# Performance work log

Hardware: AMD Instinct MI355X
Metric: run time of the kernel (lower is better)

The kernel has to match this reference:

```python
import jax, jax.numpy as jnp
import numpy as np

C = 256
CQK = C // 8


def setup_inputs() -> dict:
    key = jax.random.key(0)
    ks = jax.random.split(key, 8)
    B, H, W = 4, 64, 64
    inputs = jax.random.normal(ks[0], (B, H, W, C), dtype=jnp.float32)
    s = 1.0 / np.sqrt(C)
    Wq = jax.random.normal(ks[1], (C, CQK), dtype=jnp.float32) * s
    bq = jnp.zeros((CQK,), dtype=jnp.float32)
    Wk = jax.random.normal(ks[2], (C, CQK), dtype=jnp.float32) * s
    bk = jnp.zeros((CQK,), dtype=jnp.float32)
    Wv = jax.random.normal(ks[3], (C, C), dtype=jnp.float32) * s
    bv = jnp.zeros((C,), dtype=jnp.float32)
    gamma = jnp.float32(0.7)  # nonzero so attention branch contributes
    return {"inputs": inputs, "Wq": Wq, "bq": bq, "Wk": Wk, "bk": bk,
            "Wv": Wv, "bv": bv, "gamma": gamma}


def reference(inputs, Wq, bq, Wk, bk, Wv, bv, gamma):
    B, H, W, Cin = inputs.shape
    N = H * W
    x = inputs.reshape(B, N, Cin)
    # 1x1 convs == per-pixel channel matmuls
    q = x @ Wq + bq                      # (B, N, C//8)
    k = x @ Wk + bk                      # (B, N, C//8)
    v = x @ Wv + bv                      # (B, N, C)
    energy = jnp.einsum('bnd,bmd->bnm', q, k)   # (B, N, N), no scale (faithful)
    attn = jax.nn.softmax(energy, axis=-1)
    x_out = jnp.einsum('bnm,bmc->bnc', attn, v)  # (B, N, C)
    out = gamma * x_out.reshape(B, H, W, Cin) + inputs
    return out
```

## Files before the change

kernel.cpp:

```cpp
#include <hip/hip_runtime.h>
#include <hip/hip_bf16.h>

#define B_ 4
#define N_ 4096
#define C_ 256
#define D_ 32
#define LOG2E 1.44269504088896340736f
#define MFMA16 __builtin_amdgcn_mfma_f32_16x16x32_bf16

typedef __attribute__((ext_vector_type(8))) short short8;
typedef __attribute__((ext_vector_type(4))) short short4v;
typedef __attribute__((ext_vector_type(4))) float float4v;

__device__ inline short f2bf_rne(float f) {
  unsigned u = __builtin_bit_cast(unsigned, f);
  u += 0x7FFFu + ((u >> 16) & 1u);
  return (short)(u >> 16);
}
__device__ inline float bf2f(short s) {
  unsigned u = ((unsigned)(unsigned short)s) << 16;
  return __builtin_bit_cast(float, u);
}
__device__ inline float fast_exp2(float x) { return __builtin_amdgcn_exp2f(x); }

__global__ __launch_bounds__(256) void cast_w_kernel(
    const float* __restrict__ Wq, const float* __restrict__ Wk,
    const float* __restrict__ Wv, short* __restrict__ WtF) {
  int i  = blockIdx.x * 256 + threadIdx.x;
  int j  = i & 7;
  int l  = (i >> 3) & 63;
  int ks = (i >> 9) & 7;
  int nb = i >> 12;
  int n  = nb * 16 + (l & 15);
  int k  = ks * 32 + ((l >> 4) << 3) + j;
  float v;
  if (n < 32)      v = Wq[k * 32 + n] * LOG2E;
  else if (n < 64) v = Wk[k * 32 + (n - 32)];
  else             v = Wv[k * 256 + (n - 64)];
  WtF[i] = f2bf_rne(v);
}

__global__ __launch_bounds__(256, 2) void proj_kernel(
    const float* __restrict__ x, const short* __restrict__ WtF,
    const float* __restrict__ bq, const float* __restrict__ bk,
    const float* __restrict__ bv,
    short* __restrict__ qb, short* __restrict__ kF, short* __restrict__ vF) {
  int blk = blockIdx.x;
  int b  = blk >> 7;
  int r0 = (blk & 127) * 32;
  int t  = threadIdx.x;
  int w  = t >> 6;
  int l  = t & 63;
  int lc = l & 15;
  int q4 = l >> 4;

  __shared__ __align__(16) short sA[32][272];
  __shared__ __align__(16) short sV[256][40];
  __shared__ __align__(16) short sK[32][36];

  {
    const float* xb = x + (size_t)(b * N_ + r0) * C_;
#pragma unroll
    for (int ch = 0; ch < 8; ch++) {
      int f   = ch * 256 + t;
      int row = f >> 6;
      int col = (f & 63) * 4;
      float4v v = *(const float4v*)(xb + f * 4);
      short4v s;
      s[0] = f2bf_rne(v[0]); s[1] = f2bf_rne(v[1]);
      s[2] = f2bf_rne(v[2]); s[3] = f2bf_rne(v[3]);
      *(short4v*)(&sA[row][col]) = s;
    }
  }
  __syncthreads();

  float4v acc[10];
#pragma unroll
  for (int i = 0; i < 10; i++) { acc[i][0] = 0.f; acc[i][1] = 0.f; acc[i][2] = 0.f; acc[i][3] = 0.f; }

  const short* wbase = WtF + w * 4096 + l * 8;

#define LOADW(B0, B1, B2, B3, B4, KS)                       \
  B0 = *(const short8*)(wbase + (KS) * 512 + 0 * 16384);    \
  B1 = *(const short8*)(wbase + (KS) * 512 + 1 * 16384);    \
  B2 = *(const short8*)(wbase + (KS) * 512 + 2 * 16384);    \
  B3 = *(const short8*)(wbase + (KS) * 512 + 3 * 16384);    \
  B4 = *(const short8*)(wbase + (KS) * 512 + 4 * 16384);

#define DO_MFMA(A0, A1, B0, B1, B2, B3, B4)                 \
  acc[0] = MFMA16(A0, B0, acc[0], 0, 0, 0);                 \
  acc[1] = MFMA16(A1, B0, acc[1], 0, 0, 0);                 \
  acc[2] = MFMA16(A0, B1, acc[2], 0, 0, 0);                 \
  acc[3] = MFMA16(A1, B1, acc[3], 0, 0, 0);                 \
  acc[4] = MFMA16(A0, B2, acc[4], 0, 0, 0);                 \
  acc[5] = MFMA16(A1, B2, acc[5], 0, 0, 0);                 \
  acc[6] = MFMA16(A0, B3, acc[6], 0, 0, 0);                 \
  acc[7] = MFMA16(A1, B3, acc[7], 0, 0, 0);                 \
  acc[8] = MFMA16(A0, B4, acc[8], 0, 0, 0);                 \
  acc[9] = MFMA16(A1, B4, acc[9], 0, 0, 0);

  short8 wA0, wA1, wA2, wA3, wA4, wB0, wB1, wB2, wB3, wB4;
  LOADW(wA0, wA1, wA2, wA3, wA4, 0)
#pragma unroll
  for (int kk = 0; kk < 8; kk += 2) {
    short8 a00 = *(const short8*)(&sA[lc][kk * 32 + q4 * 8]);
    short8 a01 = *(const short8*)(&sA[16 + lc][kk * 32 + q4 * 8]);
    LOADW(wB0, wB1, wB2, wB3, wB4, kk + 1)
    DO_MFMA(a00, a01, wA0, wA1, wA2, wA3, wA4)
    short8 a10 = *(const short8*)(&sA[lc][(kk + 1) * 32 + q4 * 8]);
    short8 a11 = *(const short8*)(&sA[16 + lc][(kk + 1) * 32 + q4 * 8]);
    LOADW(wA0, wA1, wA2, wA3, wA4, kk + 2)
    DO_MFMA(a10, a11, wB0, wB1, wB2, wB3, wB4)
  }
#undef LOADW
#undef DO_MFMA

  {
    float bias0 = (w < 2) ? bq[w * 16 + lc] * LOG2E : bk[(w - 2) * 16 + lc];
#pragma unroll
    for (int rt = 0; rt < 2; rt++) {
      if (w < 2) {
#pragma unroll
        for (int r = 0; r < 4; r++) {
          int row = rt * 16 + q4 * 4 + r;
          qb[(size_t)(b * N_ + r0 + row) * D_ + w * 16 + lc] =
              f2bf_rne(acc[rt][r] + bias0);
        }
      } else {
#pragma unroll
        for (int r = 0; r < 4; r++) {
          int row = rt * 16 + q4 * 4 + r;
          sK[row][(w - 2) * 16 + lc] = f2bf_rne(acc[rt][r] + bias0);
        }
      }
    }
#pragma unroll
    for (int nbo = 1; nbo < 5; nbo++) {
      float bias = bv[(nbo - 1) * 64 + w * 16 + lc];
#pragma unroll
      for (int rt = 0; rt < 2; rt++) {
        float4v a = acc[nbo * 2 + rt];
        short4v pk;
        pk[0] = f2bf_rne(a[0] + bias); pk[1] = f2bf_rne(a[1] + bias);
        pk[2] = f2bf_rne(a[2] + bias); pk[3] = f2bf_rne(a[3] + bias);
        *(short4v*)(&sV[(nbo - 1) * 64 + w * 16 + lc][rt * 16 + q4 * 4]) = pk;
      }
    }
  }
  __syncthreads();

  int kt  = r0 >> 6;
  int ks0 = (r0 >> 5) & 1;

  {
    size_t tb2 = ((size_t)(b * 64 + kt) * 32 + ks0 * 16) * 512;
    int cb = t >> 4;
#pragma unroll
    for (int k = 0; k < 4; k++) {
      int p = (t & 15) * 4 + k;
      int j = p >> 4, i = p & 15;
      short8 vv = *(const short8*)(&sV[cb * 16 + i][j * 8]);
      *(short8*)(vF + tb2 + (size_t)t * 32 + k * 8) = vv;
    }
  }
  if (t < 128) {
    int fr = t >> 6, ll = t & 63;
    int kv = fr * 16 + (ll & 15), dg = ll >> 4;
    size_t tbk = ((size_t)(b * 64 + kt) * 4 + ks0 * 2) * 512;
    short8 kv8 = *(const short8*)(&sK[kv][dg * 8]);
    *(short8*)(kF + tbk + (size_t)t * 8) = kv8;
  }
}

__global__ __launch_bounds__(512, 4) void flash_partial_kernel(
    const short* __restrict__ qb, const short* __restrict__ kF,
    const short* __restrict__ vF, short* __restrict__ obuf,
    float* __restrict__ lbuf) {
  int blk = blockIdx.x;
  int b  = blk & 3;
  int hb = (blk >> 2) & 1;
  int qt = blk >> 3;
  int r0 = qt * 64;
  int t  = threadIdx.x;
  int w  = t >> 6;
  int l  = t & 63;
  int lc = l & 15;
  int q4 = l >> 4;
  int rq = w & 3;
  bool qkw = (w < 4);

  __shared__ __align__(16) short sP[2][64][72];

  int p = (b * 64 + qt) * 2 + hb;

  short8 qf = *(const short8*)(qb + (size_t)(b * N_ + r0 + rq * 16 + lc) * D_ + q4 * 8);

  const short* kbp = kF + ((size_t)(b * 64 + hb * 32) * 4) * 512 + l * 8;
  const short* vbp = vF + ((size_t)(b * 64 + hb * 32) * 32 + 2 * w) * 512 + l * 8;

  short8 kC0, kC1, kC2, kC3;
  short8 vX00, vX01, vX10, vX11;
  short8 vY00, vY01, vY10, vY11;

  kC0 = *(const short8*)(kbp + 0);
  kC1 = *(const short8*)(kbp + 512);
  kC2 = *(const short8*)(kbp + 1024);
  kC3 = *(const short8*)(kbp + 1536);
  vX00 = *(const short8*)(vbp + 0);
  vX01 = *(const short8*)(vbp + 512);
  vX10 = *(const short8*)(vbp + 8192);
  vX11 = *(const short8*)(vbp + 8704);

  float4v O[8];
#pragma unroll
  for (int i = 0; i < 8; i++) { O[i][0] = 0.f; O[i][1] = 0.f; O[i][2] = 0.f; O[i][3] = 0.f; }
  float l_part = 0.f;

#define K_RELOAD(TI)                                                           \
  { size_t o_ = (size_t)(TI) * 2048;                                           \
    kC0 = *(const short8*)(kbp + o_);                                          \
    kC1 = *(const short8*)(kbp + o_ + 512);                                    \
    kC2 = *(const short8*)(kbp + o_ + 1024);                                   \
    kC3 = *(const short8*)(kbp + o_ + 1536); }

#define QK_STEP(SPB, VALID)                                                    \
  { float4v z; z[0] = 0.f; z[1] = 0.f; z[2] = 0.f; z[3] = 0.f;                 \
    float4v S0 = MFMA16(kC0, qf, z, 0, 0, 0);                                  \
    float4v S1 = MFMA16(kC1, qf, z, 0, 0, 0);                                  \
    float4v S2 = MFMA16(kC2, qf, z, 0, 0, 0);                                  \
    float4v S3 = MFMA16(kC3, qf, z, 0, 0, 0);                                  \
    short* rowp = &sP[SPB][rq * 16 + lc][q4 * 4];                              \
    float ts = 0.f;                                                            \
    { float p0 = fast_exp2(S0[0]), p1 = fast_exp2(S0[1]);                      \
      float p2 = fast_exp2(S0[2]), p3 = fast_exp2(S0[3]);                      \
      ts += (p0 + p1) + (p2 + p3);                                             \
      short4v pk; pk[0] = f2bf_rne(p0); pk[1] = f2bf_rne(p1);                  \
      pk[2] = f2bf_rne(p2); pk[3] = f2bf_rne(p3);                              \
      *(short4v*)(rowp + 0) = pk; }                                            \
    { float p0 = fast_exp2(S1[0]), p1 = fast_exp2(S1[1]);                      \
      float p2 = fast_exp2(S1[2]), p3 = fast_exp2(S1[3]);                      \
      ts += (p0 + p1) + (p2 + p3);                                             \
      short4v pk; pk[0] = f2bf_rne(p0); pk[1] = f2bf_rne(p1);                  \
      pk[2] = f2bf_rne(p2); pk[3] = f2bf_rne(p3);                              \
      *(short4v*)(rowp + 16) = pk; }                                           \
    { float p0 = fast_exp2(S2[0]), p1 = fast_exp2(S2[1]);                      \
      float p2 = fast_exp2(S2[2]), p3 = fast_exp2(S2[3]);                      \
      ts += (p0 + p1) + (p2 + p3);                                             \
      short4v pk; pk[0] = f2bf_rne(p0); pk[1] = f2bf_rne(p1);                  \
      pk[2] = f2bf_rne(p2); pk[3] = f2bf_rne(p3);                              \
      *(short4v*)(rowp + 32) = pk; }                                           \
    { float p0 = fast_exp2(S3[0]), p1 = fast_exp2(S3[1]);                      \
      float p2 = fast_exp2(S3[2]), p3 = fast_exp2(S3[3]);                      \
      ts += (p0 + p1) + (p2 + p3);                                             \
      short4v pk; pk[0] = f2bf_rne(p0); pk[1] = f2bf_rne(p1);                  \
      pk[2] = f2bf_rne(p2); pk[3] = f2bf_rne(p3);                              \
      *(short4v*)(rowp + 48) = pk; }                                           \
    if (VALID) l_part += ts; }

#define PV_STEP(SPB, V00, V01, V10, V11)                                       \
  { _Pragma("unroll")                                                          \
    for (int rt = 0; rt < 4; rt++) {                                           \
      short8 pf0 = *(const short8*)(&sP[SPB][rt * 16 + lc][q4 * 8]);           \
      short8 pf1 = *(const short8*)(&sP[SPB][rt * 16 + lc][32 + q4 * 8]);      \
      O[rt * 2 + 0] = MFMA16(pf0, V00, O[rt * 2 + 0], 0, 0, 0);                \
      O[rt * 2 + 0] = MFMA16(pf1, V10, O[rt * 2 + 0], 0, 0, 0);                \
      O[rt * 2 + 1] = MFMA16(pf0, V01, O[rt * 2 + 1], 0, 0, 0);                \
      O[rt * 2 + 1] = MFMA16(pf1, V11, O[rt * 2 + 1], 0, 0, 0);                \
    } }

  if (qkw) {
    QK_STEP(0, true)
    K_RELOAD(1)
  }
  __syncthreads();

  for (int ti = 0; ti < 32; ti += 2) {
    int n1 = ti + 1;
    int n2 = (ti + 2 < 32) ? ti + 2 : 31;
    bool v2 = (ti + 2 < 32);
    int n3 = (ti + 3 < 32) ? ti + 3 : 31;

    { size_t vo = (size_t)n1 * 16384;
      vY00 = *(const short8*)(vbp + vo);
      vY01 = *(const short8*)(vbp + vo + 512);
      vY10 = *(const short8*)(vbp + vo + 8192);
      vY11 = *(const short8*)(vbp + vo + 8704); }
    if (qkw) {
      QK_STEP(1, true)
      K_RELOAD(n2)
    }
    PV_STEP(0, vX00, vX01, vX10, vX11)
    __syncthreads();

    { size_t vo = (size_t)n2 * 16384;
      vX00 = *(const short8*)(vbp + vo);
      vX01 = *(const short8*)(vbp + vo + 512);
      vX10 = *(const short8*)(vbp + vo + 8192);
      vX11 = *(const short8*)(vbp + vo + 8704); }
    if (qkw) {
      QK_STEP(0, v2)
      K_RELOAD(n3)
    }
    PV_STEP(1, vY00, vY01, vY10, vY11)
    __syncthreads();
  }
#undef K_RELOAD
#undef QK_STEP
#undef PV_STEP

  {
    short* ob = obuf + ((size_t)p * 64 + w * 8) * 256 + l * 4;
#pragma unroll
    for (int a = 0; a < 8; a++) {
      float4v o = O[a];
      short4v pk;
      pk[0] = f2bf_rne(o[0]); pk[1] = f2bf_rne(o[1]);
      pk[2] = f2bf_rne(o[2]); pk[3] = f2bf_rne(o[3]);
      *(short4v*)(ob + a * 256) = pk;
    }
  }
  if (qkw) {
    float l_tot = l_part + __shfl_xor(l_part, 16, 64);
    l_tot += __shfl_xor(l_tot, 32, 64);
    if (q4 == 0) lbuf[(size_t)p * 64 + rq * 16 + lc] = l_tot;
  }
}

__global__ __launch_bounds__(256) void merge_kernel(
    const short* __restrict__ obuf, const float* __restrict__ lbuf,
    const float* __restrict__ xin, const float* __restrict__ gptr,
    float* __restrict__ out) {
  int blk = blockIdx.x;
  int t   = threadIdx.x;
  float g = *gptr;

  __shared__ float sS[32][260];
  __shared__ float sLinv[64];

  const short* o0 = obuf + (size_t)(blk * 2 + 0) * 16384;
  const short* o1 = obuf + (size_t)(blk * 2 + 1) * 16384;
  const float* l0 = lbuf + (size_t)(blk * 2 + 0) * 64;
  const float* l1 = lbuf + (size_t)(blk * 2 + 1) * 64;
  size_t gbase = (size_t)blk * 16384;

  if (t < 64) sLinv[t] = __builtin_amdgcn_rcpf(l0[t] + l1[t]);

#pragma unroll
  for (int h = 0; h < 2; h++) {
#pragma unroll
    for (int j = 0; j < 4; j++) {
      int gdx    = j * 256 + t;
      int chunk  = gdx >> 7;
      int within = gdx & 127;
      int offs   = (chunk * 8 + 4 * h) * 256 + within * 8;
      short8 a8 = *(const short8*)(o0 + offs);
      short8 c8 = *(const short8*)(o1 + offs);
      int s_in  = within >> 5;
      int pos8  = within & 31;
      int rt    = 2 * h + (s_in >> 1);
      int cbo   = s_in & 1;
      int chB   = chunk * 32 + cbo * 16;
#pragma unroll
      for (int e = 0; e < 8; e++) {
        int lane = pos8 * 2 + (e >> 2);
        int r    = e & 3;
        int row  = (rt & 1) * 16 + (lane >> 4) * 4 + r;
        int ch   = chB + (lane & 15);
        sS[row][ch] = bf2f(a8[e]) + bf2f(c8[e]);
      }
    }
    __syncthreads();

#pragma unroll
    for (int j = 0; j < 8; j++) {
      int gdx = j * 1024 + t * 4;
      int row = 32 * h + (gdx >> 8);
      int ch  = gdx & 255;
      float linv = sLinv[row];
      size_t gi = gbase + (size_t)(32 * h) * 256 + gdx;
      float4v xv = *(const float4v*)(xin + gi);
      float4v sv = *(const float4v*)(&sS[row - 32 * h][ch]);
      float4v ov;
#pragma unroll
      for (int e = 0; e < 4; e++) ov[e] = g * (sv[e] * linv) + xv[e];
      *(float4v*)(out + gi) = ov;
    }
    __syncthreads();
  }
}

extern "C" void kernel_launch(void* const* d_in, const int* in_sizes, int n_in,
                              void* d_out, int out_size, void* d_ws, size_t ws_size,
                              hipStream_t stream) {
  const float* x     = (const float*)d_in[0];
  const float* Wq    = (const float*)d_in[1];
  const float* bq    = (const float*)d_in[2];
  const float* Wk    = (const float*)d_in[3];
  const float* bk    = (const float*)d_in[4];
  const float* Wv    = (const float*)d_in[5];
  const float* bv    = (const float*)d_in[6];
  const float* gamma = (const float*)d_in[7];
  float* out = (float*)d_out;

  char* ws = (char*)d_ws;
  short* qb   = (short*)ws;
  short* kF   = (short*)(ws + (1u << 20));
  short* vF   = (short*)(ws + (2u << 20));
  short* WtF  = (short*)(ws + (10u << 20));
  short* obuf = (short*)(ws + (11u << 20));
  float* lbuf = (float*)(ws + (28u << 20));

  hipLaunchKernelGGL(cast_w_kernel,        dim3(320), dim3(256), 0, stream, Wq, Wk, Wv, WtF);
  hipLaunchKernelGGL(proj_kernel,          dim3(512), dim3(256), 0, stream, x, WtF, bq, bk, bv, qb, kF, vF);
  hipLaunchKernelGGL(flash_partial_kernel, dim3(512), dim3(512), 0, stream, qb, kF, vF, obuf, lbuf);
  hipLaunchKernelGGL(merge_kernel,         dim3(256), dim3(256), 0, stream, obuf, lbuf, x, gamma, out);
}
```

Measured before the change: 142.1 us.

## Specialize warps into QK/softmax producers and PV consumers

Splits the 8 waves so waves 0-3 only compute QK scores, exp and the row sums into shared memory, while waves 4-7 only do the PV MFMAs over 64 output channels each (16 accumulators instead of 8). V loads move entirely to the consumer waves and the output layout in obuf changes, so the merge kernel's indexing is updated to match. The aim is to let the softmax/QK work and the PV matmul run concurrently on different waves rather than serialised inside every wave. The cost is doubled accumulator registers in the consumer waves, which can raise register pressure under the 512x4 launch bounds, and a possible load imbalance between the two groups.

```diff
diff --git a/kernel.cpp b/kernel.cpp
--- a/kernel.cpp
+++ b/kernel.cpp
@@ -187,6 +187,7 @@
   int lc = l & 15;
   int q4 = l >> 4;
   int rq = w & 3;
+  int cq = w & 3;
   bool qkw = (w < 4);
 
   __shared__ __align__(16) short sP[2][64][72];
@@ -196,24 +197,27 @@
   short8 qf = *(const short8*)(qb + (size_t)(b * N_ + r0 + rq * 16 + lc) * D_ + q4 * 8);
 
   const short* kbp = kF + ((size_t)(b * 64 + hb * 32) * 4) * 512 + l * 8;
-  const short* vbp = vF + ((size_t)(b * 64 + hb * 32) * 32 + 2 * w) * 512 + l * 8;
+  const short* vbp = vF + ((size_t)(b * 64 + hb * 32) * 32 + cq * 4) * 512 + l * 8;
 
   short8 kC0, kC1, kC2, kC3;
-  short8 vX00, vX01, vX10, vX11;
-  short8 vY00, vY01, vY10, vY11;
-
-  kC0 = *(const short8*)(kbp + 0);
-  kC1 = *(const short8*)(kbp + 512);
-  kC2 = *(const short8*)(kbp + 1024);
-  kC3 = *(const short8*)(kbp + 1536);
-  vX00 = *(const short8*)(vbp + 0);
-  vX01 = *(const short8*)(vbp + 512);
-  vX10 = *(const short8*)(vbp + 8192);
-  vX11 = *(const short8*)(vbp + 8704);
-
-  float4v O[8];
-#pragma unroll
-  for (int i = 0; i < 8; i++) { O[i][0] = 0.f; O[i][1] = 0.f; O[i][2] = 0.f; O[i][3] = 0.f; }
+  short8 vC[8];
+
+  if (qkw) {
+    kC0 = *(const short8*)(kbp + 0);
+    kC1 = *(const short8*)(kbp + 512);
+    kC2 = *(const short8*)(kbp + 1024);
+    kC3 = *(const short8*)(kbp + 1536);
+  } else {
+#pragma unroll
+    for (int ks = 0; ks < 2; ks++)
+#pragma unroll
+      for (int cb = 0; cb < 4; cb++)
+        vC[ks * 4 + cb] = *(const short8*)(vbp + ks * 8192 + cb * 512);
+  }
+
+  float4v O[16];
+#pragma unroll
+  for (int i = 0; i < 16; i++) { O[i][0] = 0.f; O[i][1] = 0.f; O[i][2] = 0.f; O[i][3] = 0.f; }
   float l_part = 0.f;
 
 #define K_RELOAD(TI)                                                           \
@@ -222,6 +226,14 @@
     kC1 = *(const short8*)(kbp + o_ + 512);                                    \
     kC2 = *(const short8*)(kbp + o_ + 1024);                                   \
     kC3 = *(const short8*)(kbp + o_ + 1536); }
+
+#define V_RELOAD(TI)                                                           \
+  { size_t vo = (size_t)(TI) * 16384;                                          \
+    _Pragma("unroll")                                                          \
+    for (int ks = 0; ks < 2; ks++)                                             \
+      _Pragma("unroll")                                                        \
+      for (int cb = 0; cb < 4; cb++)                                           \
+        vC[ks * 4 + cb] = *(const short8*)(vbp + vo + ks * 8192 + cb * 512); }
 
 #define QK_STEP(SPB, VALID)                                                    \
   { float4v z; z[0] = 0.f; z[1] = 0.f; z[2] = 0.f; z[3] = 0.f;                 \
@@ -257,15 +269,16 @@
       *(short4v*)(rowp + 48) = pk; }                                           \
     if (VALID) l_part += ts; }
 
-#define PV_STEP(SPB, V00, V01, V10, V11)                                       \
+#define PV_STEP(SPB)                                                           \
   { _Pragma("unroll")                                                          \
     for (int rt = 0; rt < 4; rt++) {                                           \
       short8 pf0 = *(const short8*)(&sP[SPB][rt * 16 + lc][q4 * 8]);           \
       short8 pf1 = *(const short8*)(&sP[SPB][rt * 16 + lc][32 + q4 * 8]);      \
-      O[rt * 2 + 0] = MFMA16(pf0, V00, O[rt * 2 + 0], 0, 0, 0);                \
-      O[rt * 2 + 0] = MFMA16(pf1, V10, O[rt * 2 + 0], 0, 0, 0);                \
-      O[rt * 2 + 1] = MFMA16(pf0, V01, O[rt * 2 + 1], 0, 0, 0);                \
-      O[rt * 2 + 1] = MFMA16(pf1, V11, O[rt * 2 + 1], 0, 0, 0);                \
+      _Pragma("unroll")                                                        \
+      for (int cb = 0; cb < 4; cb++) {                                         \
+        O[rt * 4 + cb] = MFMA16(pf0, vC[cb],     O[rt * 4 + cb], 0, 0, 0);     \
+        O[rt * 4 + cb] = MFMA16(pf1, vC[4 + cb], O[rt * 4 + cb], 0, 0, 0);     \
+      }                                                                        \
     } }
 
   if (qkw) {
@@ -280,46 +293,40 @@
     bool v2 = (ti + 2 < 32);
     int n3 = (ti + 3 < 32) ? ti + 3 : 31;
 
-    { size_t vo = (size_t)n1 * 16384;
-      vY00 = *(const short8*)(vbp + vo);
-      vY01 = *(const short8*)(vbp + vo + 512);
-      vY10 = *(const short8*)(vbp + vo + 8192);
-      vY11 = *(const short8*)(vbp + vo + 8704); }
     if (qkw) {
       QK_STEP(1, true)
       K_RELOAD(n2)
-    }
-    PV_STEP(0, vX00, vX01, vX10, vX11)
+    } else {
+      PV_STEP(0)
+      V_RELOAD(n1)
+    }
     __syncthreads();
 
-    { size_t vo = (size_t)n2 * 16384;
-      vX00 = *(const short8*)(vbp + vo);
-      vX01 = *(const short8*)(vbp + vo + 512);
-      vX10 = *(const short8*)(vbp + vo + 8192);
-      vX11 = *(const short8*)(vbp + vo + 8704); }
     if (qkw) {
       QK_STEP(0, v2)
       K_RELOAD(n3)
-    }
-    PV_STEP(1, vY00, vY01, vY10, vY11)
+    } else {
+      PV_STEP(1)
+      V_RELOAD(n2)
+    }
     __syncthreads();
   }
 #undef K_RELOAD
+#undef V_RELOAD
 #undef QK_STEP
 #undef PV_STEP
 
-  {
-    short* ob = obuf + ((size_t)p * 64 + w * 8) * 256 + l * 4;
-#pragma unroll
-    for (int a = 0; a < 8; a++) {
+  if (!qkw) {
+    short* ob = obuf + ((size_t)p * 64 + cq * 16) * 256 + l * 4;
+#pragma unroll
+    for (int a = 0; a < 16; a++) {
       float4v o = O[a];
       short4v pk;
       pk[0] = f2bf_rne(o[0]); pk[1] = f2bf_rne(o[1]);
       pk[2] = f2bf_rne(o[2]); pk[3] = f2bf_rne(o[3]);
       *(short4v*)(ob + a * 256) = pk;
     }
-  }
-  if (qkw) {
+  } else {
     float l_tot = l_part + __shfl_xor(l_part, 16, 64);
     l_tot += __shfl_xor(l_tot, 32, 64);
     if (q4 == 0) lbuf[(size_t)p * 64 + rq * 16 + lc] = l_tot;
@@ -349,22 +356,22 @@
   for (int h = 0; h < 2; h++) {
 #pragma unroll
     for (int j = 0; j < 4; j++) {
-      int gdx    = j * 256 + t;
-      int chunk  = gdx >> 7;
-      int within = gdx & 127;
-      int offs   = (chunk * 8 + 4 * h) * 256 + within * 8;
+      int gdx  = j * 256 + t;
+      int ucq  = gdx >> 8;
+      int rem  = gdx & 255;
+      int jj   = rem >> 5;
+      int pos8 = rem & 31;
+      int offs = (ucq * 16 + h * 8 + jj) * 256 + pos8 * 8;
       short8 a8 = *(const short8*)(o0 + offs);
       short8 c8 = *(const short8*)(o1 + offs);
-      int s_in  = within >> 5;
-      int pos8  = within & 31;
-      int rt    = 2 * h + (s_in >> 1);
-      int cbo   = s_in & 1;
-      int chB   = chunk * 32 + cbo * 16;
+      int rtl = jj >> 2;
+      int cb  = jj & 3;
+      int chB = ucq * 64 + cb * 16;
 #pragma unroll
       for (int e = 0; e < 8; e++) {
         int lane = pos8 * 2 + (e >> 2);
         int r    = e & 3;
-        int row  = (rt & 1) * 16 + (lane >> 4) * 4 + r;
+        int row  = rtl * 16 + (lane >> 4) * 4 + r;
         int ch   = chB + (lane & 15);
         sS[row][ch] = bf2f(a8[e]) + bf2f(c8[e]);
       }
```

Result: slower. 156.0 us (+9.8%).
